# Kernel optimization log

Hardware: AMD Instinct MI355X
Metric: run time of the kernel (lower is better)

Reference implementation:

```python
import jax, jax.numpy as jnp
import numpy as np

N = 8192       # num nodes
NFEAT = 512    # input feature dim
NHID = 128     # hidden dim (GraphConvolution in/out_features)
NCLASS = 40    # output classes
LAM0 = 1.0
LAM1 = 1.0
ALPHA = 1.0 / (1.0 + LAM0 + LAM1)  # args.alp == 0 path
STEPS = 8      # args.prop_step


def setup_inputs() -> dict:
    key = jax.random.key(0)
    ks = jax.random.split(key, 9)
    x = jax.random.normal(ks[0], (N, NFEAT), jnp.float32)
    # dense (normalized) hypergraph adjacencies; scale ~1/N so row sums stay O(1)
    A_beta = jax.random.uniform(ks[1], (N, N), jnp.float32) * (1.0 / N)
    A_gamma = jax.random.uniform(ks[2], (N, N), jnp.float32) * (1.0 / N)
    # diagonal degree operators D_beta, D_gamma (stored as vectors)
    d_beta = jax.random.uniform(ks[3], (N,), jnp.float32)
    d_gamma = jax.random.uniform(ks[4], (N,), jnp.float32)
    eye = jnp.eye(NHID, dtype=jnp.float32)
    # H params init: N(0, 1/in_features) + I  (notresidual=False branch)
    H1 = jax.random.normal(ks[5], (NHID, NHID), jnp.float32) * (1.0 / NHID) + eye
    H2 = jax.random.normal(ks[6], (NHID, NHID), jnp.float32) * (1.0 / NHID) + eye
    W1 = jax.random.normal(ks[7], (NHID, NFEAT), jnp.float32) * (1.0 / np.sqrt(NFEAT))
    b1 = jnp.zeros((NHID,), jnp.float32)
    W2 = jax.random.normal(ks[8], (NCLASS, NHID), jnp.float32) * (1.0 / np.sqrt(NHID))
    b2 = jnp.zeros((NCLASS,), jnp.float32)
    return dict(x=x, A_beta=A_beta, A_gamma=A_gamma, d_beta=d_beta, d_gamma=d_gamma,
                H1=H1, H2=H2, W1=W1, b1=b1, W2=W2, b2=b2)


def reference(x, A_beta, A_gamma, d_beta, d_gamma, H1, H2, W1, b1, W2, b2):
    # phenomnn (eval mode => dropout is identity): fc1 -> relu -> GraphConvolution -> relu -> fc2
    Y0 = jax.nn.relu(x @ W1.T + b1)                      # [N, NHID]
    # Q_tild = lam0*D_beta + lam1*D_gamma + I (diagonal); precompute its inverse
    q_inv = 1.0 / (LAM0 * d_beta + LAM1 * d_gamma + 1.0)  # [N]
    S1 = H1 + H1.T
    P1 = H1 @ H1.T
    S2 = H2 + H2.T
    P2 = H2 @ H2.T
    db = d_beta[:, None]
    dg = d_gamma[:, None]

    def step(Y, _):
        AbY = A_beta @ Y                                  # [N, NHID]
        AgY = A_gamma @ Y
        # L_gamma @ Y = (D_gamma - A_gamma) @ Y = dg*Y - AgY
        Y_hat = (LAM0 * (AbY @ S1 - db * (Y @ P1))
                 + Y0
                 + LAM1 * ((dg * Y - AgY) + AgY @ S2 - dg * (Y @ P2)))
        Y_new = (1.0 - ALPHA) * Y + ALPHA * (q_inv[:, None] * Y_hat)
        return Y_new, None

    Y, _ = jax.lax.scan(step, Y0, None, length=STEPS)
    Y = jax.nn.relu(Y)
    return Y @ W2.T + b2                                  # [N, NCLASS]
```

## Files before the change

kernel.cpp:

```cpp
#include <hip/hip_runtime.h>
#include <hip/hip_bf16.h>
#include <stdint.h>

#define LAM0 1.0f
#define LAM1 1.0f
#define ALPHA_F (1.0f/3.0f)

typedef unsigned short u16;
typedef unsigned char u8;
typedef __attribute__((ext_vector_type(4))) float f32x4;
typedef __attribute__((ext_vector_type(16))) float f32x16;
typedef __attribute__((ext_vector_type(8))) __bf16 bf16x8;
typedef __attribute__((ext_vector_type(8))) int i32x8;

__device__ __forceinline__ u16 f2bfu(float f){
  union { __hip_bfloat16 h; u16 u; } cv;
  cv.h = __float2bfloat16(f);
  return cv.u;
}

__device__ __forceinline__ unsigned int pk4_fp8(float a, float b, float c, float d){
  int w = 0;
  w = __builtin_amdgcn_cvt_pk_fp8_f32(a, b, w, false);
  w = __builtin_amdgcn_cvt_pk_fp8_f32(c, d, w, true);
  return (unsigned int)w;
}

__device__ __forceinline__ void async16(void* lds, const void* g){
  __builtin_amdgcn_global_load_lds((const __attribute__((address_space(1))) void*)g,
                                   (__attribute__((address_space(3))) void*)lds, 16, 0, 0);
}

__global__ void prep_bsmall(const float* __restrict__ H1, const float* __restrict__ H2,
                            u16* __restrict__ BsT){
  int np = blockIdx.x;
  int k  = threadIdx.x;
  float v;
  if (np < 128){
    v = LAM0*(H1[k*128+np] + H1[np*128+k]);
  } else if (np < 256){
    int j = np-128;
    v = LAM1*(H2[k*128+j] + H2[j*128+k] - (k==j ? 1.0f : 0.0f));
  } else if (np < 384){
    int j = np-256; float s = 0.f;
    for (int q=0;q<128;++q) s += H1[k*128+q]*H1[j*128+q];
    v = s;
  } else {
    int j = np-384; float s = 0.f;
    for (int q=0;q<128;++q) s += H2[k*128+q]*H2[j*128+q];
    v = s;
  }
  BsT[np*128+k] = f2bfu(v);
}

__global__ void qinv_kernel(const float* __restrict__ db, const float* __restrict__ dg,
                            float* __restrict__ q){
  int i = blockIdx.x*256 + threadIdx.x;
  if (i < 8192) q[i] = 1.0f/(LAM0*db[i] + LAM1*dg[i] + 1.0f);
}

__global__ void cast_simple(const float* __restrict__ s, u16* __restrict__ d, int n){
  int i = blockIdx.x*256 + threadIdx.x;
  if (i < n) d[i] = f2bfu(s[i]);
}

__global__ void cast_acat8(const float* __restrict__ Ab, const float* __restrict__ Ag,
                           u8* __restrict__ Acat){
  size_t o = ((size_t)blockIdx.x*256 + threadIdx.x)*16;
  size_t i = o >> 14;
  int k = (int)(o & 16383);
  const float* src = (k < 8192) ? (Ab + i*8192 + k) : (Ag + i*8192 + (k - 8192));
  const float S = 65536.0f;
  uint4 pk;
  {
    f32x4 v0 = *(const f32x4*)(src +  0);
    f32x4 v1 = *(const f32x4*)(src +  4);
    f32x4 v2 = *(const f32x4*)(src +  8);
    f32x4 v3 = *(const f32x4*)(src + 12);
    pk.x = pk4_fp8(v0[0]*S, v0[1]*S, v0[2]*S, v0[3]*S);
    pk.y = pk4_fp8(v1[0]*S, v1[1]*S, v1[2]*S, v1[3]*S);
    pk.z = pk4_fp8(v2[0]*S, v2[1]*S, v2[2]*S, v2[3]*S);
    pk.w = pk4_fp8(v3[0]*S, v3[1]*S, v3[2]*S, v3[3]*S);
  }
  *(uint4*)(Acat + o) = pk;
}

template<int WM, int WN, int MT, int NT, int EPI>
__launch_bounds__(256, 2)
__global__ void gemm_bf16(const u16* __restrict__ A, int ldA,
                          const u16* __restrict__ B, int ldB,
                          int ksteps,
                          float* __restrict__ out0,
                          u16* __restrict__ outbf,
                          u8* __restrict__ out8,
                          const float* __restrict__ bias){
  constexpr int BM = WM*MT*16;
  constexpr int BN = WN*NT*16;
  __shared__ u16 ldsA[BM*64];
  __shared__ u16 ldsB[BN*64];
  const int tid  = threadIdx.x;
  const int m0   = blockIdx.x * BM;
  const int n0   = blockIdx.y * BN;
  const int wave = tid >> 6, lane = tid & 63;
  const int l15 = lane & 15, quad = lane >> 4;
  const int wm = wave / WN, wn = wave % WN;

  f32x4 acc[MT][NT];
  #pragma unroll
  for (int mt=0; mt<MT; ++mt)
    #pragma unroll
    for (int nt=0; nt<NT; ++nt)
      acc[mt][nt] = f32x4{0.f,0.f,0.f,0.f};

  #pragma unroll 1
  for (int it=0; it<ksteps; ++it){
    const int k0 = it*64;
    #pragma unroll
    for (int r=0; r<BM/32; ++r){
      int cid = r*256 + tid;
      int row = cid >> 3, cph = cid & 7;
      int cgl = cph ^ (row & 7);
      async16(&ldsA[cid*8], A + (size_t)(m0+row)*ldA + (k0 + cgl*8));
    }
    #pragma unroll
    for (int r=0; r<BN/32; ++r){
      int cid = r*256 + tid;
      int row = cid >> 3, cph = cid & 7;
      int cgl = cph ^ (row & 7);
      async16(&ldsB[cid*8], B + (size_t)(n0+row)*ldB + (k0 + cgl*8));
    }
    __syncthreads();
    #pragma unroll
    for (int kk=0; kk<2; ++kk){
      bf16x8 af[MT], bg[NT];
      #pragma unroll
      for (int mt=0; mt<MT; ++mt){
        int am = wm*MT*16 + mt*16 + l15;
        int cph = (kk*4 + quad) ^ (am & 7);
        af[mt] = *(const bf16x8*)&ldsA[am*64 + cph*8];
      }
      #pragma unroll
      for (int nt=0; nt<NT; ++nt){
        int bn = wn*NT*16 + nt*16 + l15;
        int cph = (kk*4 + quad) ^ (bn & 7);
        bg[nt] = *(const bf16x8*)&ldsB[bn*64 + cph*8];
      }
      #pragma unroll
      for (int mt=0; mt<MT; ++mt)
        #pragma unroll
        for (int nt=0; nt<NT; ++nt)
          acc[mt][nt] = __builtin_amdgcn_mfma_f32_16x16x32_bf16(af[mt], bg[nt], acc[mt][nt], 0, 0, 0);
    }
    __syncthreads();
  }

  const int ibase = m0 + wm*MT*16;
  const int jbase = n0 + wn*NT*16;
  if constexpr (EPI == 1){
    #pragma unroll
    for (int mt=0; mt<MT; ++mt){
      int i0 = ibase + mt*16 + quad*4;
      #pragma unroll
      for (int nt=0; nt<NT; ++nt){
        int j = jbase + nt*16 + l15;
        float bj = bias[j];
        #pragma unroll
        for (int r=0; r<4; ++r){
          float v = acc[mt][nt][r] + bj;
          v = fmaxf(v, 0.0f);
          out0 [(size_t)(i0+r)*128 + j] = v;
          outbf[(size_t)(i0+r)*128 + j] = f2bfu(v);
        }
      }
    }
  } else {
    #pragma unroll
    for (int mt=0; mt<MT; ++mt){
      int i0 = ibase + mt*16 + quad*4;
      #pragma unroll
      for (int nt=0; nt<NT; ++nt){
        int jg = jbase + nt*16 + l15;
        if (jg < 256){
          int nn = jg & 127;
          size_t koff = (jg < 128) ? (size_t)0 : (size_t)8192;
          unsigned int pk = pk4_fp8(acc[mt][nt][0], acc[mt][nt][1], acc[mt][nt][2], acc[mt][nt][3]);
          *(unsigned int*)&out8[(size_t)nn*16384 + koff + i0] = pk;
        } else {
          #pragma unroll
          for (int r=0; r<4; ++r)
            out0[(size_t)(i0+r)*256 + (jg-256)] = acc[mt][nt][r];
        }
      }
    }
  }
}

__launch_bounds__(256, 2)
__global__ void gemm_a8(const u8* __restrict__ A, const u8* __restrict__ B,
                        int ksteps, float* __restrict__ part){
  __shared__ u8 ldsA[128*128];
  __shared__ u8 ldsB[128*128];
  const int tid = threadIdx.x;
  const int m0  = blockIdx.x * 128;
  const int kch = blockIdx.z;
  const int kbase = kch * ksteps * 128;
  const int wave = tid >> 6, lane = tid & 63;
  const int l31 = lane & 31, half = lane >> 5;
  const int wm = wave >> 1, wn = wave & 1;

  f32x16 acc[2][2];
  #pragma unroll
  for (int mt=0; mt<2; ++mt)
    #pragma unroll
    for (int nt=0; nt<2; ++nt)
      #pragma unroll
      for (int r=0; r<16; ++r)
        acc[mt][nt][r] = 0.f;

  #pragma unroll 1
  for (int it=0; it<ksteps; ++it){
    const int k0 = kbase + it*128;
    #pragma unroll
    for (int r=0; r<4; ++r){
      int cid = r*256 + tid;
      int row = cid >> 3, cph = cid & 7;
      int cgl = cph ^ (row & 7);
      async16(&ldsA[cid*16], A + (size_t)(m0+row)*16384 + (k0 + cgl*16));
    }
    #pragma unroll
    for (int r=0; r<4; ++r){
      int cid = r*256 + tid;
      int row = cid >> 3, cph = cid & 7;
      int cgl = cph ^ (row & 7);
      async16(&ldsB[cid*16], B + (size_t)row*16384 + (k0 + cgl*16));
    }
    __syncthreads();
    #pragma unroll
    for (int s=0; s<2; ++s){
      const int lc = s*4 + half*2;
      i32x8 af[2], bg[2];
      #pragma unroll
      for (int mt=0; mt<2; ++mt){
        int am = wm*64 + mt*32 + l31;
        int c0 = (lc  ) ^ (am & 7);
        int c1 = (lc+1) ^ (am & 7);
        int4 lo = *(const int4*)&ldsA[am*128 + c0*16];
        int4 hi = *(const int4*)&ldsA[am*128 + c1*16];
        af[mt] = i32x8{lo.x, lo.y, lo.z, lo.w, hi.x, hi.y, hi.z, hi.w};
      }
      #pragma unroll
      for (int nt=0; nt<2; ++nt){
        int bn = wn*64 + nt*32 + l31;
        int c0 = (lc  ) ^ (bn & 7);
        int c1 = (lc+1) ^ (bn & 7);
        int4 lo = *(const int4*)&ldsB[bn*128 + c0*16];
        int4 hi = *(const int4*)&ldsB[bn*128 + c1*16];
        bg[nt] = i32x8{lo.x, lo.y, lo.z, lo.w, hi.x, hi.y, hi.z, hi.w};
      }
      #pragma unroll
      for (int mt=0; mt<2; ++mt)
        #pragma unroll
        for (int nt=0; nt<2; ++nt)
          acc[mt][nt] = __builtin_amdgcn_mfma_scale_f32_32x32x64_f8f6f4(
              af[mt], bg[nt], acc[mt][nt], 0, 0, 0, 0x7F7F7F7F, 0, 0x7F7F7F7F);
    }
    __syncthreads();
  }

  float* outp = part + (size_t)kch * (8192*128);
  #pragma unroll
  for (int mt=0; mt<2; ++mt){
    int ib = m0 + wm*64 + mt*32 + 4*half;
    #pragma unroll
    for (int nt=0; nt<2; ++nt){
      int j = wn*64 + nt*32 + l31;
      #pragma unroll
      for (int reg=0; reg<16; ++reg){
        int ri = (reg & 3) + 8*(reg >> 2);
        outp[(size_t)(ib+ri)*128 + j] = acc[mt][nt][reg] * 0x1p-16f;
      }
    }
  }
}

__global__ void step_update(const float* __restrict__ part, const float* __restrict__ Y,
                            const float* __restrict__ Y0, const float* __restrict__ UP,
                            const float* __restrict__ dbt, const float* __restrict__ dgt,
                            const float* __restrict__ qv,
                            float* __restrict__ Yn, u16* __restrict__ Ybn){
  int idx = blockIdx.x*256 + threadIdx.x;
  int e = idx*4;
  int i = e >> 7, j = e & 127;
  f32x4 g = *(const f32x4*)(part + e);
  #pragma unroll
  for (int c=1; c<8; ++c)
    g += *(const f32x4*)(part + (size_t)c*1048576 + e);
  f32x4 y  = *(const f32x4*)(Y  + e);
  f32x4 y0 = *(const f32x4*)(Y0 + e);
  f32x4 u1 = *(const f32x4*)(UP + (size_t)i*256 + j);
  f32x4 u2 = *(const f32x4*)(UP + (size_t)i*256 + 128 + j);
  float db = LAM0*dbt[i], dg = LAM1*dgt[i], qi = qv[i];
  f32x4 yh = g + y0 + dg*y - (db*u1 + dg*u2);
  f32x4 yn = (1.0f-ALPHA_F)*y + (ALPHA_F*qi)*yh;
  *(f32x4*)(Yn + e) = yn;
  ushort4 pk;
  pk.x = f2bfu(yn[0]); pk.y = f2bfu(yn[1]); pk.z = f2bfu(yn[2]); pk.w = f2bfu(yn[3]);
  *(ushort4*)(Ybn + e) = pk;
}

__global__ void final_out(const float* __restrict__ Y, const float* __restrict__ W2,
                          const float* __restrict__ b2, float* __restrict__ out){
  int g = blockIdx.x*256 + threadIdx.x;
  if (g >= 8192*40) return;
  int i = g / 40, c = g - i*40;
  const float* yr = Y + (size_t)i*128;
  const float* wr = W2 + c*128;
  float s = 0.f;
  #pragma unroll 8
  for (int k=0; k<128; k+=4){
    f32x4 yv = *(const f32x4*)(yr+k);
    f32x4 wv = *(const f32x4*)(wr+k);
    s += fmaxf(yv[0],0.f)*wv[0] + fmaxf(yv[1],0.f)*wv[1]
       + fmaxf(yv[2],0.f)*wv[2] + fmaxf(yv[3],0.f)*wv[3];
  }
  out[g] = s + b2[c];
}

extern "C" void kernel_launch(void* const* d_in, const int* in_sizes, int n_in,
                              void* d_out, int out_size, void* d_ws, size_t ws_size,
                              hipStream_t stream){
  const float* x  = (const float*)d_in[0];
  const float* Ab = (const float*)d_in[1];
  const float* Ag = (const float*)d_in[2];
  const float* db = (const float*)d_in[3];
  const float* dg = (const float*)d_in[4];
  const float* H1 = (const float*)d_in[5];
  const float* H2 = (const float*)d_in[6];
  const float* W1 = (const float*)d_in[7];
  const float* b1 = (const float*)d_in[8];
  const float* W2 = (const float*)d_in[9];
  const float* b2 = (const float*)d_in[10];
  float* out = (float*)d_out;

  char* w = (char*)d_ws;
  size_t off = 0;
  auto take = [&](size_t bytes){ void* p = w + off; off += (bytes + 255) & ~(size_t)255; return p; };
  u8*    Acat8 = (u8*)   take((size_t)8192*16384);
  u8*    Ucat8 = (u8*)   take((size_t)128*16384);
  float* UPf   = (float*)take((size_t)8192*256*4);
  float* part  = (float*)take((size_t)8*8192*128*4);
  float* Y0f   = (float*)take((size_t)8192*128*4);
  float* Ya    = (float*)take((size_t)8192*128*4);
  float* Yb    = (float*)take((size_t)8192*128*4);
  u16*   Ybf0  = (u16*)  take((size_t)8192*128*2);
  u16*   Ybfa  = (u16*)  take((size_t)8192*128*2);
  u16*   Ybfb  = (u16*)  take((size_t)8192*128*2);
  u16*   xbf   = (u16*)  take((size_t)8192*512*2);
  u16*   BsT   = (u16*)  take((size_t)512*128*2);
  u16*   W1bf  = (u16*)  take((size_t)128*512*2);
  float* qinv  = (float*)take((size_t)8192*4);
  if (off > ws_size) return;

  prep_bsmall<<<512, 128, 0, stream>>>(H1, H2, BsT);
  qinv_kernel<<<32, 256, 0, stream>>>(db, dg, qinv);
  cast_simple<<<256, 256, 0, stream>>>(W1, W1bf, 128*512);
  cast_simple<<<16384, 256, 0, stream>>>(x, xbf, 8192*512);
  cast_acat8<<<32768, 256, 0, stream>>>(Ab, Ag, Acat8);

  gemm_bf16<1,4,2,2,1><<<dim3(256,1,1), 256, 0, stream>>>(xbf, 512, W1bf, 512, 8, Y0f, Ybf0, nullptr, b1);

  const float* Yc = Y0f; const u16* Ybc = Ybf0;
  for (int s=0; s<8; ++s){
    gemm_bf16<2,2,2,4,2><<<dim3(128,4,1), 256, 0, stream>>>(Ybc, 128, BsT, 128, 2, UPf, nullptr, Ucat8, nullptr);
    gemm_a8<<<dim3(64,1,8), 256, 0, stream>>>(Acat8, Ucat8, 16, part);
    float* Yn  = (s & 1) ? Yb   : Ya;
    u16*   Ybn = (s & 1) ? Ybfb : Ybfa;
    step_update<<<1024, 256, 0, stream>>>(part, Yc, Y0f, UPf, db, dg, qinv, Yn, Ybn);
    Yc = Yn; Ybc = Ybn;
  }
  final_out<<<1280, 256, 0, stream>>>(Yc, W2, b2, out);
}
```

Baseline: 968.7 us.

## Double-buffer LDS in fp8 adjacency GEMM and widen fp8 cast per thread

The fp8 adjacency GEMM now uses two LDS buffers. It issues async global-to-LDS loads for the next K tile before computing on the current one, and drops one barrier per iteration. This aims to overlap the large streaming read of the concatenated adjacency with MFMA work. The cost is doubled LDS (64KB per block), which may limit occupancy. Separately, the one-time fp32-to-fp8 adjacency cast handles 32 elements per thread instead of 16, with half as many blocks.

Measured after the change: 956.9 us. About the same (-1.2%).

```diff
diff --git a/kernel.cpp b/kernel.cpp
--- a/kernel.cpp
+++ b/kernel.cpp
@@ -66,23 +66,32 @@
 
 __global__ void cast_acat8(const float* __restrict__ Ab, const float* __restrict__ Ag,
                            u8* __restrict__ Acat){
-  size_t o = ((size_t)blockIdx.x*256 + threadIdx.x)*16;
+  size_t o = ((size_t)blockIdx.x*256 + threadIdx.x)*32;
   size_t i = o >> 14;
   int k = (int)(o & 16383);
   const float* src = (k < 8192) ? (Ab + i*8192 + k) : (Ag + i*8192 + (k - 8192));
   const float S = 65536.0f;
-  uint4 pk;
+  uint4 p0, p1;
   {
     f32x4 v0 = *(const f32x4*)(src +  0);
     f32x4 v1 = *(const f32x4*)(src +  4);
     f32x4 v2 = *(const f32x4*)(src +  8);
     f32x4 v3 = *(const f32x4*)(src + 12);
-    pk.x = pk4_fp8(v0[0]*S, v0[1]*S, v0[2]*S, v0[3]*S);
-    pk.y = pk4_fp8(v1[0]*S, v1[1]*S, v1[2]*S, v1[3]*S);
-    pk.z = pk4_fp8(v2[0]*S, v2[1]*S, v2[2]*S, v2[3]*S);
-    pk.w = pk4_fp8(v3[0]*S, v3[1]*S, v3[2]*S, v3[3]*S);
-  }
-  *(uint4*)(Acat + o) = pk;
+    f32x4 v4 = *(const f32x4*)(src + 16);
+    f32x4 v5 = *(const f32x4*)(src + 20);
+    f32x4 v6 = *(const f32x4*)(src + 24);
+    f32x4 v7 = *(const f32x4*)(src + 28);
+    p0.x = pk4_fp8(v0[0]*S, v0[1]*S, v0[2]*S, v0[3]*S);
+    p0.y = pk4_fp8(v1[0]*S, v1[1]*S, v1[2]*S, v1[3]*S);
+    p0.z = pk4_fp8(v2[0]*S, v2[1]*S, v2[2]*S, v2[3]*S);
+    p0.w = pk4_fp8(v3[0]*S, v3[1]*S, v3[2]*S, v3[3]*S);
+    p1.x = pk4_fp8(v4[0]*S, v4[1]*S, v4[2]*S, v4[3]*S);
+    p1.y = pk4_fp8(v5[0]*S, v5[1]*S, v5[2]*S, v5[3]*S);
+    p1.z = pk4_fp8(v6[0]*S, v6[1]*S, v6[2]*S, v6[3]*S);
+    p1.w = pk4_fp8(v7[0]*S, v7[1]*S, v7[2]*S, v7[3]*S);
+  }
+  *(uint4*)(Acat + o)      = p0;
+  *(uint4*)(Acat + o + 16) = p1;
 }
 
 template<int WM, int WN, int MT, int NT, int EPI>
@@ -198,8 +207,8 @@
 __launch_bounds__(256, 2)
 __global__ void gemm_a8(const u8* __restrict__ A, const u8* __restrict__ B,
                         int ksteps, float* __restrict__ part){
-  __shared__ u8 ldsA[128*128];
-  __shared__ u8 ldsB[128*128];
+  __shared__ u8 ldsA[2][128*128];
+  __shared__ u8 ldsB[2][128*128];
   const int tid = threadIdx.x;
   const int m0  = blockIdx.x * 128;
   const int kch = blockIdx.z;
@@ -208,33 +217,40 @@
   const int l31 = lane & 31, half = lane >> 5;
   const int wm = wave >> 1, wn = wave & 1;
 
-  f32x16 acc[2][2];
-  #pragma unroll
-  for (int mt=0; mt<2; ++mt)
-    #pragma unroll
-    for (int nt=0; nt<2; ++nt)
-      #pragma unroll
-      for (int r=0; r<16; ++r)
-        acc[mt][nt][r] = 0.f;
-
-  #pragma unroll 1
-  for (int it=0; it<ksteps; ++it){
+  auto stage = [&](int buf, int it){
     const int k0 = kbase + it*128;
     #pragma unroll
     for (int r=0; r<4; ++r){
       int cid = r*256 + tid;
       int row = cid >> 3, cph = cid & 7;
       int cgl = cph ^ (row & 7);
-      async16(&ldsA[cid*16], A + (size_t)(m0+row)*16384 + (k0 + cgl*16));
+      async16(&ldsA[buf][cid*16], A + (size_t)(m0+row)*16384 + (k0 + cgl*16));
     }
     #pragma unroll
     for (int r=0; r<4; ++r){
       int cid = r*256 + tid;
       int row = cid >> 3, cph = cid & 7;
       int cgl = cph ^ (row & 7);
-      async16(&ldsB[cid*16], B + (size_t)row*16384 + (k0 + cgl*16));
-    }
+      async16(&ldsB[buf][cid*16], B + (size_t)row*16384 + (k0 + cgl*16));
+    }
+  };
+
+  f32x16 acc[2][2];
+  #pragma unroll
+  for (int mt=0; mt<2; ++mt)
+    #pragma unroll
+    for (int nt=0; nt<2; ++nt)
+      #pragma unroll
+      for (int r=0; r<16; ++r)
+        acc[mt][nt][r] = 0.f;
+
+  stage(0, 0);
+  #pragma unroll 1
+  for (int it=0; it<ksteps; ++it){
     __syncthreads();
+    if (it+1 < ksteps) stage((it+1)&1, it+1);
+    const u8* lA = ldsA[it&1];
+    const u8* lB = ldsB[it&1];
     #pragma unroll
     for (int s=0; s<2; ++s){
       const int lc = s*4 + half*2;
@@ -244,8 +260,8 @@
         int am = wm*64 + mt*32 + l31;
         int c0 = (lc  ) ^ (am & 7);
         int c1 = (lc+1) ^ (am & 7);
-        int4 lo = *(const int4*)&ldsA[am*128 + c0*16];
-        int4 hi = *(const int4*)&ldsA[am*128 + c1*16];
+        int4 lo = *(const int4*)&lA[am*128 + c0*16];
+        int4 hi = *(const int4*)&lA[am*128 + c1*16];
         af[mt] = i32x8{lo.x, lo.y, lo.z, lo.w, hi.x, hi.y, hi.z, hi.w};
       }
       #pragma unroll
@@ -253,8 +269,8 @@
         int bn = wn*64 + nt*32 + l31;
         int c0 = (lc  ) ^ (bn & 7);
         int c1 = (lc+1) ^ (bn & 7);
-        int4 lo = *(const int4*)&ldsB[bn*128 + c0*16];
-        int4 hi = *(const int4*)&ldsB[bn*128 + c1*16];
+        int4 lo = *(const int4*)&lB[bn*128 + c0*16];
+        int4 hi = *(const int4*)&lB[bn*128 + c1*16];
         bg[nt] = i32x8{lo.x, lo.y, lo.z, lo.w, hi.x, hi.y, hi.z, hi.w};
       }
       #pragma unroll
@@ -264,7 +280,6 @@
           acc[mt][nt] = __builtin_amdgcn_mfma_scale_f32_32x32x64_f8f6f4(
               af[mt], bg[nt], acc[mt][nt], 0, 0, 0, 0x7F7F7F7F, 0, 0x7F7F7F7F);
     }
-    __syncthreads();
   }
 
   float* outp = part + (size_t)kch * (8192*128);
@@ -365,7 +380,7 @@
   qinv_kernel<<<32, 256, 0, stream>>>(db, dg, qinv);
   cast_simple<<<256, 256, 0, stream>>>(W1, W1bf, 128*512);
   cast_simple<<<16384, 256, 0, stream>>>(x, xbf, 8192*512);
-  cast_acat8<<<32768, 256, 0, stream>>>(Ab, Ag, Acat8);
+  cast_acat8<<<16384, 256, 0, stream>>>(Ab, Ag, Acat8);
 
   gemm_bf16<1,4,2,2,1><<<dim3(256,1,1), 256, 0, stream>>>(xbf, 512, W1bf, 512, 8, Y0f, Ybf0, nullptr, b1);
 
```
